# Kernel tuning notes

Measured on AMD Instinct MI355X. Metric: run time of the kernel, lower is better.

The kernel has to match this reference:

```python
import jax, jax.numpy as jnp
import numpy as np
from jax import lax

VOCAB, EMB, HID, TAGS = 8000, 300, 512, 24  # hidden_dim=512 -> 256 per direction
B, S = 128, 512
H2 = HID // 2


def setup_inputs() -> dict:
    key = jax.random.key(0)
    ks = jax.random.split(key, 16)
    sc = 0.05
    inp = {
        "chars": jax.random.randint(ks[0], (B, S), 0, VOCAB),
        "tags": jax.random.randint(ks[1], (B, S), 0, TAGS),
        "mask": jnp.ones((B, S), dtype=bool),
        "emb": jax.random.normal(ks[2], (VOCAB, EMB), jnp.float32) * sc,
        # PyTorch LSTM layout: gates stacked [i, f, g, o]
        "w_ih_f": jax.random.normal(ks[3], (4 * H2, EMB), jnp.float32) * sc,
        "w_hh_f": jax.random.normal(ks[4], (4 * H2, H2), jnp.float32) * sc,
        "b_f": jax.random.normal(ks[5], (4 * H2,), jnp.float32) * sc,  # b_ih + b_hh fused
        "w_ih_b": jax.random.normal(ks[6], (4 * H2, EMB), jnp.float32) * sc,
        "w_hh_b": jax.random.normal(ks[7], (4 * H2, H2), jnp.float32) * sc,
        "b_b": jax.random.normal(ks[8], (4 * H2,), jnp.float32) * sc,
        "w_out": jax.random.normal(ks[9], (TAGS, HID), jnp.float32) * sc,
        "b_out": jax.random.normal(ks[10], (TAGS,), jnp.float32) * sc,
        "trans": jax.random.normal(ks[11], (TAGS, TAGS), jnp.float32) * sc,
        "start_trans": jax.random.normal(ks[12], (TAGS,), jnp.float32) * sc,
        "end_trans": jax.random.normal(ks[13], (TAGS,), jnp.float32) * sc,
    }
    return inp


def _lstm_dir(x, w_ih, w_hh, b, reverse):
    # x: [B, S, E] -> h: [B, S, H2]
    gx = jnp.einsum('bse,ge->bsg', x, w_ih) + b  # [B, S, 4*H2]

    def step(carry, g_t):
        h, c = carry
        g = g_t + h @ w_hh.T
        i, f, gg, o = jnp.split(g, 4, axis=-1)
        c = jax.nn.sigmoid(f) * c + jax.nn.sigmoid(i) * jnp.tanh(gg)
        h = jax.nn.sigmoid(o) * jnp.tanh(c)
        return (h, c), h

    init = (jnp.zeros((x.shape[0], H2), x.dtype), jnp.zeros((x.shape[0], H2), x.dtype))
    _, hs = lax.scan(step, init, jnp.swapaxes(gx, 0, 1), reverse=reverse)
    return jnp.swapaxes(hs, 0, 1)


def _crf_loss(emissions, tags, mask, trans, start_trans, end_trans):
    # torchcrf log-likelihood, reduction='mean'; loss = -mean
    b, s, t = emissions.shape
    maskf = mask.astype(emissions.dtype)
    # numerator: score of gold path
    em_t = jnp.take_along_axis(emissions, tags[..., None], axis=2)[..., 0]  # [B,S]
    tr_t = trans[tags[:, :-1], tags[:, 1:]]  # [B,S-1]
    score = start_trans[tags[:, 0]] + em_t[:, 0]
    score = score + jnp.sum((em_t[:, 1:] + tr_t) * maskf[:, 1:], axis=1)
    seq_ends = jnp.sum(mask.astype(jnp.int32), axis=1) - 1  # [B]
    last_tags = jnp.take_along_axis(tags, seq_ends[:, None], axis=1)[:, 0]
    score = score + end_trans[last_tags]
    # denominator: forward algorithm via scan
    alpha0 = start_trans + emissions[:, 0]  # [B,T]

    def step(alpha, inputs):
        em, m = inputs  # em [B,T], m [B]
        nxt = jax.nn.logsumexp(alpha[:, :, None] + trans[None] + em[:, None, :], axis=1)
        alpha = jnp.where(m[:, None], nxt, alpha)
        return alpha, None

    alpha, _ = lax.scan(step, alpha0,
                        (jnp.swapaxes(emissions[:, 1:], 0, 1), jnp.swapaxes(mask[:, 1:], 0, 1)))
    log_z = jax.nn.logsumexp(alpha + end_trans, axis=1)  # [B]
    llh = score - log_z
    return -jnp.mean(llh)


def reference(chars, tags, mask, emb, w_ih_f, w_hh_f, b_f, w_ih_b, w_hh_b, b_b,
              w_out, b_out, trans, start_trans, end_trans):
    x = emb[chars]  # [B,S,E]
    h_f = _lstm_dir(x, w_ih_f, w_hh_f, b_f, reverse=False)
    h_b = _lstm_dir(x, w_ih_b, w_hh_b, b_b, reverse=True)
    lstm_out = jnp.concatenate([h_f, h_b], axis=-1)  # [B,S,HID]
    emissions = jnp.einsum('bsh,th->bst', lstm_out, w_out) + b_out  # [B,S,TAGS]
    return _crf_loss(emissions, tags, mask, trans, start_trans, end_trans)
```

## Files before the change

kernel.cpp:

```cpp
#include <hip/hip_runtime.h>
#include <math.h>

#define BB   128
#define SS   512
#define EMBD 300
#define VOC  8000
#define NTAG 24
#define BSD  (BB*SS)

#define SW   400.0f
#define SH   512.0f
#define INVQ (1.0f / (400.0f * 512.0f))

typedef unsigned int   u32;
typedef unsigned short u16;
typedef unsigned char  u8;

__device__ __forceinline__ int idot4(u32 a, u32 b, int c) {
#if __has_builtin(__builtin_amdgcn_sdot4)
    return __builtin_amdgcn_sdot4((int)a, (int)b, c, false);
#else
    int s = c;
    #pragma unroll
    for (int e = 0; e < 4; ++e) {
        int xa = ((int)(a << (24 - 8 * e))) >> 24;
        int xb = ((int)(b << (24 - 8 * e))) >> 24;
        s += xa * xb;
    }
    return s;
#endif
}
__device__ __forceinline__ u32 rdlane(u32 v, int l) {
#if __has_builtin(__builtin_amdgcn_readlane)
    return (u32)__builtin_amdgcn_readlane((int)v, l);
#else
    return (u32)__shfl((int)v, l);
#endif
}
__device__ __forceinline__ void bar_lds() {
    asm volatile("s_waitcnt lgkmcnt(0)" ::: "memory");
    __builtin_amdgcn_s_barrier();
}
__device__ __forceinline__ float sigm(float x) { return 1.0f / (1.0f + __expf(-x)); }
__device__ __forceinline__ float tanh_fast(float x) {
    return 1.0f - 2.0f / (__expf(2.0f * x) + 1.0f);
}
__device__ __forceinline__ int qclamp(float x, float s) {
    int v = (int)rintf(x * s);
    return v > 127 ? 127 : (v < -127 ? -127 : v);
}
__device__ __forceinline__ u32 q4(const float* p, float s) {
    u32 r = 0;
    #pragma unroll
    for (int e = 0; e < 4; ++e)
        r |= ((u32)(qclamp(p[e], s) & 0xFF)) << (8 * e);
    return r;
}

__global__ __launch_bounds__(512)
void k_packW(const float* __restrict__ w_hh_f, const float* __restrict__ w_hh_b,
             const float* __restrict__ w_out,
             u32* __restrict__ wreg, uint4* __restrict__ wlds,
             uint4* __restrict__ wstr, u32* __restrict__ woq)
{
    const int dir = blockIdx.x;
    const int t   = threadIdx.x;
    const float* w = dir ? w_hh_b : w_hh_f;
    const float* rowA = w + (size_t)t * 256;
    const float* rowB = w + (size_t)(t + 512) * 256;

    for (int q = 0; q < 16; ++q) {
        wreg[((size_t)(dir * 32 + q) * 512) + t]      = q4(rowA + 4 * q, SW);
        wreg[((size_t)(dir * 32 + 16 + q) * 512) + t] = q4(rowB + 4 * q, SW);
    }
    for (int qq = 0; qq < 7; ++qq) {
        uint4 va, vb;
        va.x = q4(rowA + 4 * (16 + 4 * qq + 0), SW);
        va.y = q4(rowA + 4 * (16 + 4 * qq + 1), SW);
        va.z = q4(rowA + 4 * (16 + 4 * qq + 2), SW);
        va.w = q4(rowA + 4 * (16 + 4 * qq + 3), SW);
        vb.x = q4(rowB + 4 * (16 + 4 * qq + 0), SW);
        vb.y = q4(rowB + 4 * (16 + 4 * qq + 1), SW);
        vb.z = q4(rowB + 4 * (16 + 4 * qq + 2), SW);
        vb.w = q4(rowB + 4 * (16 + 4 * qq + 3), SW);
        wlds[((size_t)(dir * 14 + qq) * 512) + t]     = va;
        wlds[((size_t)(dir * 14 + 7 + qq) * 512) + t] = vb;
    }
    for (int qq = 0; qq < 5; ++qq) {
        uint4 va, vb;
        va.x = q4(rowA + 4 * (44 + 4 * qq + 0), SW);
        va.y = q4(rowA + 4 * (44 + 4 * qq + 1), SW);
        va.z = q4(rowA + 4 * (44 + 4 * qq + 2), SW);
        va.w = q4(rowA + 4 * (44 + 4 * qq + 3), SW);
        vb.x = q4(rowB + 4 * (44 + 4 * qq + 0), SW);
        vb.y = q4(rowB + 4 * (44 + 4 * qq + 1), SW);
        vb.z = q4(rowB + 4 * (44 + 4 * qq + 2), SW);
        vb.w = q4(rowB + 4 * (44 + 4 * qq + 3), SW);
        wstr[((size_t)(dir * 10 + qq) * 512) + t]     = va;
        wstr[((size_t)(dir * 10 + 5 + qq) * 512) + t] = vb;
    }
    for (int i = t; i < NTAG * 64; i += 512) {
        const int tag = i >> 6, q = i & 63;
        woq[(size_t)dir * NTAG * 64 + i] =
            q4(w_out + (size_t)tag * 512 + dir * 256 + 4 * q, SW);
    }
}

__global__ __launch_bounds__(256)
void k_gxtab(const float* __restrict__ emb,
             const float* __restrict__ w_f, const float* __restrict__ bias_f,
             const float* __restrict__ w_b, const float* __restrict__ bias_b,
             u16* __restrict__ gxtab)
{
    const int dir = blockIdx.z;
    const float* W    = dir ? w_b    : w_f;
    const float* bias = dir ? bias_b : bias_f;
    u16* out = gxtab + (size_t)dir * VOC * 1024;
    const int r0 = blockIdx.y * 64;
    const int c0 = blockIdx.x * 128;

    __shared__ float As[16][65];
    __shared__ float Bs[16][129];

    const int tid = threadIdx.x;
    const int kk = tid & 15;
    const int rr = tid >> 4;
    const int ty = tid >> 4;
    const int tx = tid & 15;

    float acc[4][8] = {};

    for (int kt = 0; kt < EMBD; kt += 16) {
        const int k = kt + kk;
        const bool kok = (k < EMBD);
        #pragma unroll
        for (int p = 0; p < 4; ++p)
            As[kk][rr + p * 16] = kok ? emb[(size_t)(r0 + rr + p * 16) * EMBD + k] : 0.0f;
        #pragma unroll
        for (int p = 0; p < 8; ++p)
            Bs[kk][rr + p * 16] = kok ? W[(size_t)(c0 + rr + p * 16) * EMBD + k] : 0.0f;
        __syncthreads();
        #pragma unroll
        for (int q = 0; q < 16; ++q) {
            float av[4], bv[8];
            #pragma unroll
            for (int i = 0; i < 4; ++i) av[i] = As[q][ty * 4 + i];
            #pragma unroll
            for (int jj = 0; jj < 8; ++jj) bv[jj] = Bs[q][jj * 16 + tx];
            #pragma unroll
            for (int i = 0; i < 4; ++i)
                #pragma unroll
                for (int jj = 0; jj < 8; ++jj)
                    acc[i][jj] = fmaf(av[i], bv[jj], acc[i][jj]);
        }
        __syncthreads();
    }

    #pragma unroll
    for (int i = 0; i < 4; ++i) {
        const size_t rb = (size_t)(r0 + ty * 4 + i) * 1024;
        #pragma unroll
        for (int jj = 0; jj < 8; ++jj) {
            const int cl = c0 + jj * 16 + tx;
            out[rb + cl] = __builtin_bit_cast(u16, (_Float16)(acc[i][jj] + bias[cl]));
        }
    }
}

__global__ __launch_bounds__(512, 2)
void k_lstm_rl(const int* __restrict__ chars, const u16* __restrict__ gxtab,
               const u32* __restrict__ wreg, const uint4* __restrict__ wlds,
               const uint4* __restrict__ wstr,
               u32* __restrict__ hst)
{
    const int bid = blockIdx.x;
    const int dir = bid >> 7;
    const int b   = bid & 127;
    const int tid = threadIdx.x;

    __shared__ __align__(16) uint4 ldsW[14 * 512];
    __shared__ __align__(16) u32   hq[2][64];
    __shared__ __align__(16) float2 xg[256];
    __shared__ int chlds[SS];

    chlds[tid] = chars[(size_t)b * SS + tid];
    {
        const uint4* wl = wlds + (size_t)dir * 14 * 512;
        #pragma unroll
        for (int q = 0; q < 14; ++q) ldsW[q * 512 + tid] = wl[(size_t)q * 512 + tid];
    }

    u32 WR[32];
    {
        const u32* wrp = wreg + (size_t)dir * 32 * 512 + tid;
        #pragma unroll
        for (int q = 0; q < 32; ++q) WR[q] = wrp[(size_t)q * 512];
    }
    const uint4* wsp = wstr + (size_t)dir * 10 * 512 + tid;

    const u16* gxp = gxtab + (size_t)dir * VOC * 1024;

    float c = 0.0f;
    u32 hreg = 0u;
    __syncthreads();

    const int t0 = dir ? (SS - 1) : 0;
    u16 gA = gxp[(size_t)chlds[t0] * 1024 + tid];
    u16 gB = gxp[(size_t)chlds[t0] * 1024 + 512 + tid];

    int cur = 0;
    #pragma unroll 1
    for (int sloc = 0; sloc < SS; ++sloc) {
        const int t = dir ? (SS - 1 - sloc) : sloc;

        u16 gA_n = 0, gB_n = 0;
        if (sloc < SS - 1) {
            const int tn = dir ? (t - 1) : (t + 1);
            const size_t o = (size_t)chlds[tn] * 1024 + tid;
            gA_n = gxp[o];
            gB_n = gxp[o + 512];
        }
        uint4 s[10];
        #pragma unroll
        for (int qq = 0; qq < 10; ++qq) s[qq] = wsp[(size_t)qq * 512];

        int aA = 0, aB = 0;
        #pragma unroll
        for (int q = 0; q < 16; ++q) {
            const u32 hs = rdlane(hreg, q);
            aA = idot4(WR[q], hs, aA);
            aB = idot4(WR[16 + q], hs, aB);
        }
        #pragma unroll
        for (int qq = 0; qq < 7; ++qq) {
            const uint4 wa = ldsW[qq * 512 + tid];
            const uint4 wb = ldsW[(7 + qq) * 512 + tid];
            const u32 h0 = rdlane(hreg, 16 + 4 * qq + 0);
            const u32 h1 = rdlane(hreg, 16 + 4 * qq + 1);
            const u32 h2 = rdlane(hreg, 16 + 4 * qq + 2);
            const u32 h3 = rdlane(hreg, 16 + 4 * qq + 3);
            aA = idot4(wa.x, h0, aA); aB = idot4(wb.x, h0, aB);
            aA = idot4(wa.y, h1, aA); aB = idot4(wb.y, h1, aB);
            aA = idot4(wa.z, h2, aA); aB = idot4(wb.z, h2, aB);
            aA = idot4(wa.w, h3, aA); aB = idot4(wb.w, h3, aB);
        }
        #pragma unroll
        for (int qq = 0; qq < 5; ++qq) {
            const uint4 wa = s[qq];
            const uint4 wb = s[5 + qq];
            const u32 h0 = rdlane(hreg, 44 + 4 * qq + 0);
            const u32 h1 = rdlane(hreg, 44 + 4 * qq + 1);
            const u32 h2 = rdlane(hreg, 44 + 4 * qq + 2);
            const u32 h3 = rdlane(hreg, 44 + 4 * qq + 3);
            aA = idot4(wa.x, h0, aA); aB = idot4(wb.x, h0, aB);
            aA = idot4(wa.y, h1, aA); aB = idot4(wb.y, h1, aB);
            aA = idot4(wa.z, h2, aA); aB = idot4(wb.z, h2, aB);
            aA = idot4(wa.w, h3, aA); aB = idot4(wb.w, h3, aB);
        }
        const float apreA = (float)aA * INVQ + (float)__builtin_bit_cast(_Float16, gA);
        const float apreB = (float)aB * INVQ + (float)__builtin_bit_cast(_Float16, gB);

        if (tid >= 256) xg[tid - 256] = make_float2(sigm(apreA), sigm(apreB));
        bar_lds();

        if (tid < 256) {
            const float2 fo = xg[tid];
            const float ig = sigm(apreA);
            const float gg = tanh_fast(apreB);
            c = fmaf(fo.x, c, ig * gg);
            const float h = fo.y * tanh_fast(c);
            const int hi = qclamp(h, SH);
            ((u8*)hq[cur ^ 1])[tid] = (u8)(hi & 0xFF);
        }
        bar_lds();

        hreg = hq[cur ^ 1][tid & 63];
        if (tid < 64)
            hst[(((size_t)b * SS + t) * 2 + dir) * 64 + tid] = hreg;

        gA = gA_n; gB = gB_n;
        cur ^= 1;
    }
}

__global__ __launch_bounds__(256)
void k_emis(const u32* __restrict__ hst, const u32* __restrict__ woq,
            const float* __restrict__ b_out, float* __restrict__ emis)
{
    const int r0  = blockIdx.x * 32;
    const int tid = threadIdx.x;

    __shared__ __align__(16) u32 hs[32 * 132];
    __shared__ __align__(16) u32 wo[NTAG * 132];

    #pragma unroll
    for (int p = 0; p < 16; ++p) {
        const int idx = p * 256 + tid;
        const int row = idx >> 7, rest = idx & 127;
        hs[row * 132 + rest] = hst[((size_t)(r0 + row)) * 128 + rest];
    }
    for (int i = tid; i < NTAG * 128; i += 256) {
        const int tag = i >> 7, q = i & 127;
        const u32 v = (q < 64) ? woq[tag * 64 + q]
                               : woq[NTAG * 64 + tag * 64 + (q - 64)];
        wo[tag * 132 + q] = v;
    }
    __syncthreads();

    #pragma unroll
    for (int rep = 0; rep < 3; ++rep) {
        const int out = rep * 256 + tid;
        const int row = out / 24;
        const int tag = out - row * 24;
        const uint4* h4 = (const uint4*)&hs[row * 132];
        const uint4* w4 = (const uint4*)&wo[tag * 132];
        int e = 0;
        #pragma unroll
        for (int q = 0; q < 32; ++q) {
            const uint4 hv = h4[q];
            const uint4 wv = w4[q];
            e = idot4(wv.x, hv.x, e);
            e = idot4(wv.y, hv.y, e);
            e = idot4(wv.z, hv.z, e);
            e = idot4(wv.w, hv.w, e);
        }
        emis[(size_t)(r0 + row) * NTAG + tag] = (float)e * INVQ + b_out[tag];
    }
}

__global__ __launch_bounds__(64)
void k_crf(const float* __restrict__ emis, const int* __restrict__ tags,
           const float* __restrict__ trans, const float* __restrict__ start_tr,
           const float* __restrict__ end_tr, float* __restrict__ llh)
{
    const int b    = blockIdx.x;
    const int lane = threadIdx.x;
    const float* em = emis + (size_t)b * SS * NTAG;
    const int*   tg = tags + (size_t)b * SS;
    const bool active = (lane < NTAG);

    float trans_reg[NTAG];
    #pragma unroll
    for (int i = 0; i < NTAG; ++i)
        trans_reg[i] = active ? trans[i * NTAG + lane] : 0.0f;

    float sc = 0.0f;
    for (int t = lane; t < SS; t += 64) {
        const int tt = tg[t];
        sc += em[t * NTAG + tt];
        if (t > 0) sc += trans[tg[t - 1] * NTAG + tt];
    }
    #pragma unroll
    for (int off = 32; off > 0; off >>= 1) sc += __shfl_down(sc, off);

    float alpha = active ? (start_tr[lane] + em[lane]) : -1e30f;
    for (int t = 1; t < SS; ++t) {
        float v[NTAG];
        #pragma unroll
        for (int i = 0; i < NTAG; ++i)
            v[i] = __shfl(alpha, i) + trans_reg[i];
        float m = v[0];
        #pragma unroll
        for (int i = 1; i < NTAG; ++i) m = fmaxf(m, v[i]);
        float ssum = 0.0f;
        #pragma unroll
        for (int i = 0; i < NTAG; ++i) ssum += __expf(v[i] - m);
        const float e = active ? em[t * NTAG + lane] : 0.0f;
        alpha = active ? (m + __logf(ssum) + e) : -1e30f;
    }

    float v = alpha + (active ? end_tr[lane] : 0.0f);
    float m = v;
    #pragma unroll
    for (int off = 32; off > 0; off >>= 1) m = fmaxf(m, __shfl_down(m, off));
    m = __shfl(m, 0);
    float e = __expf(v - m);
    #pragma unroll
    for (int off = 32; off > 0; off >>= 1) e += __shfl_down(e, off);

    if (lane == 0) {
        const float logz  = m + __logf(e);
        const float score = sc + start_tr[tg[0]] + end_tr[tg[SS - 1]];
        llh[b] = score - logz;
    }
}

__global__ __launch_bounds__(64)
void k_final(const float* __restrict__ llh, float* __restrict__ out)
{
    const int lane = threadIdx.x;
    float v = llh[lane] + llh[lane + 64];
    #pragma unroll
    for (int off = 32; off > 0; off >>= 1) v += __shfl_down(v, off);
    if (lane == 0) out[0] = -(v * (1.0f / 128.0f));
}

extern "C" void kernel_launch(void* const* d_in, const int* in_sizes, int n_in,
                              void* d_out, int out_size, void* d_ws, size_t ws_size,
                              hipStream_t stream)
{
    (void)in_sizes; (void)n_in; (void)out_size; (void)ws_size;

    const int*   chars   = (const int*)d_in[0];
    const int*   tags    = (const int*)d_in[1];
    const float* emb     = (const float*)d_in[3];
    const float* w_ih_f  = (const float*)d_in[4];
    const float* w_hh_f  = (const float*)d_in[5];
    const float* b_f     = (const float*)d_in[6];
    const float* w_ih_b  = (const float*)d_in[7];
    const float* w_hh_b  = (const float*)d_in[8];
    const float* b_b     = (const float*)d_in[9];
    const float* w_out   = (const float*)d_in[10];
    const float* b_out   = (const float*)d_in[11];
    const float* trans   = (const float*)d_in[12];
    const float* start_t = (const float*)d_in[13];
    const float* end_t   = (const float*)d_in[14];

    char* ws = (char*)d_ws;
    size_t off = 0;
    auto carve = [&](size_t bytes) -> char* {
        char* p = ws + off;
        off += (bytes + 255) & ~(size_t)255;
        return p;
    };
    u16*   gxtab  = (u16*)carve((size_t)2 * VOC * 1024 * 2);
    u32*   wreg   = (u32*)carve((size_t)2 * 32 * 512 * 4);
    uint4* wlds   = (uint4*)carve((size_t)2 * 14 * 512 * 16);
    uint4* wstr   = (uint4*)carve((size_t)2 * 10 * 512 * 16);
    u32*   woq    = (u32*)carve((size_t)2 * NTAG * 64 * 4);
    u32*   hst    = (u32*)carve((size_t)BSD * 2 * 64 * 4);
    float* emis   = (float*)carve((size_t)BSD * NTAG * 4);
    float* llh    = (float*)carve(128 * 4);

    hipLaunchKernelGGL(k_packW, dim3(2), dim3(512), 0, stream,
                       w_hh_f, w_hh_b, w_out, wreg, wlds, wstr, woq);
    hipLaunchKernelGGL(k_gxtab, dim3(8, 125, 2), dim3(256), 0, stream,
                       emb, w_ih_f, b_f, w_ih_b, b_b, gxtab);
    hipLaunchKernelGGL(k_lstm_rl, dim3(256), dim3(512), 0, stream,
                       chars, gxtab, wreg, wlds, wstr, hst);
    hipLaunchKernelGGL(k_emis, dim3(BSD / 32), dim3(256), 0, stream,
                       hst, woq, b_out, emis);
    hipLaunchKernelGGL(k_crf, dim3(128), dim3(64), 0, stream,
                       emis, tags, trans, start_t, end_t, llh);
    hipLaunchKernelGGL(k_final, dim3(1), dim3(64), 0, stream,
                       llh, (float*)d_out);
}
```

Measured before the change: 1.107 ms.

## Use 1024-thread LSTM blocks with one gate per thread and int8 input GEMM

The recurrent kernel moves from 512 threads computing two gate rows each to 1024 threads computing one gate row each. Each thread keeps 44 weight words in registers and reads the other 20 words from LDS, so the per-step global streaming of weights is dropped. The embedding and input-weight GEMM is rewritten to quantise inputs to int8 in a new pack kernel and accumulate with sdot4. This shortens the serial dependency chain per step and cuts the precompute cost, at the price of extra quantisation error in the input projection and heavier register and occupancy pressure.

After: 1.126 ms. No clear change (+1.7%).

```diff
diff --git a/kernel.cpp b/kernel.cpp
--- a/kernel.cpp
+++ b/kernel.cpp
@@ -8,9 +8,16 @@
 #define NTAG 24
 #define BSD  (BB*SS)
 
+#define RKG  44
+#define LKG  5
+
 #define SW   400.0f
 #define SH   512.0f
 #define INVQ (1.0f / (400.0f * 512.0f))
+
+#define SQE  440.0f
+#define INVQE (1.0f / (440.0f * 440.0f))
+#define KQ   80
 
 typedef unsigned int   u32;
 typedef unsigned short u16;
@@ -56,48 +63,54 @@
         r |= ((u32)(qclamp(p[e], s) & 0xFF)) << (8 * e);
     return r;
 }
+__device__ __forceinline__ u32 q4g(const float* p, int n, float s) {
+    u32 r = 0;
+    #pragma unroll
+    for (int e = 0; e < 4; ++e) {
+        const int v = (e < n) ? qclamp(p[e], s) : 0;
+        r |= ((u32)(v & 0xFF)) << (8 * e);
+    }
+    return r;
+}
+
+__global__ __launch_bounds__(128)
+void k_packE(const float* __restrict__ emb, const float* __restrict__ w_ih_f,
+             const float* __restrict__ w_ih_b, u32* __restrict__ eq)
+{
+    const int row = blockIdx.x;
+    const int g   = threadIdx.x;
+    if (g >= KQ) return;
+    const float* src = (row < 8000) ? (emb + (size_t)row * EMBD)
+                     : (row < 9024) ? (w_ih_f + (size_t)(row - 8000) * EMBD)
+                                    : (w_ih_b + (size_t)(row - 9024) * EMBD);
+    const int ks = g * 4;
+    const int n  = (ks >= EMBD) ? 0 : ((EMBD - ks) >= 4 ? 4 : (EMBD - ks));
+    eq[(size_t)row * KQ + g] = (n == 4) ? q4(src + ks, SQE) : q4g(src + ks, n, SQE);
+}
 
 __global__ __launch_bounds__(512)
 void k_packW(const float* __restrict__ w_hh_f, const float* __restrict__ w_hh_b,
              const float* __restrict__ w_out,
              u32* __restrict__ wreg, uint4* __restrict__ wlds,
-             uint4* __restrict__ wstr, u32* __restrict__ woq)
+             u32* __restrict__ woq)
 {
     const int dir = blockIdx.x;
     const int t   = threadIdx.x;
     const float* w = dir ? w_hh_b : w_hh_f;
-    const float* rowA = w + (size_t)t * 256;
-    const float* rowB = w + (size_t)(t + 512) * 256;
-
-    for (int q = 0; q < 16; ++q) {
-        wreg[((size_t)(dir * 32 + q) * 512) + t]      = q4(rowA + 4 * q, SW);
-        wreg[((size_t)(dir * 32 + 16 + q) * 512) + t] = q4(rowB + 4 * q, SW);
-    }
-    for (int qq = 0; qq < 7; ++qq) {
-        uint4 va, vb;
-        va.x = q4(rowA + 4 * (16 + 4 * qq + 0), SW);
-        va.y = q4(rowA + 4 * (16 + 4 * qq + 1), SW);
-        va.z = q4(rowA + 4 * (16 + 4 * qq + 2), SW);
-        va.w = q4(rowA + 4 * (16 + 4 * qq + 3), SW);
-        vb.x = q4(rowB + 4 * (16 + 4 * qq + 0), SW);
-        vb.y = q4(rowB + 4 * (16 + 4 * qq + 1), SW);
-        vb.z = q4(rowB + 4 * (16 + 4 * qq + 2), SW);
-        vb.w = q4(rowB + 4 * (16 + 4 * qq + 3), SW);
-        wlds[((size_t)(dir * 14 + qq) * 512) + t]     = va;
-        wlds[((size_t)(dir * 14 + 7 + qq) * 512) + t] = vb;
-    }
-    for (int qq = 0; qq < 5; ++qq) {
-        uint4 va, vb;
-        va.x = q4(rowA + 4 * (44 + 4 * qq + 0), SW);
-        va.y = q4(rowA + 4 * (44 + 4 * qq + 1), SW);
-        va.z = q4(rowA + 4 * (44 + 4 * qq + 2), SW);
-        va.w = q4(rowA + 4 * (44 + 4 * qq + 3), SW);
-        vb.x = q4(rowB + 4 * (44 + 4 * qq + 0), SW);
-        vb.y = q4(rowB + 4 * (44 + 4 * qq + 1), SW);
-        vb.z = q4(rowB + 4 * (44 + 4 * qq + 2), SW);
-        vb.w = q4(rowB + 4 * (44 + 4 * qq + 3), SW);
-        wstr[((size_t)(dir * 10 + qq) * 512) + t]     = va;
-        wstr[((size_t)(dir * 10 + 5 + qq) * 512) + t] = vb;
+
+    for (int half = 0; half < 2; ++half) {
+        const int r = half * 512 + t;
+        const float* row = w + (size_t)r * 256;
+        for (int q = 0; q < RKG; ++q)
+            wreg[((size_t)(dir * RKG + q) * 1024) + r] = q4(row + 4 * q, SW);
+        for (int qq = 0; qq < LKG; ++qq) {
+            uint4 v;
+            v.x = q4(row + 4 * (RKG + 4 * qq + 0), SW);
+            v.y = q4(row + 4 * (RKG + 4 * qq + 1), SW);
+            v.z = q4(row + 4 * (RKG + 4 * qq + 2), SW);
+            v.w = q4(row + 4 * (RKG + 4 * qq + 3), SW);
+            wlds[((size_t)(dir * LKG + qq) * 1024) + r] = v;
+        }
     }
     for (int i = t; i < NTAG * 64; i += 512) {
         const int tag = i >> 6, q = i & 63;
@@ -107,42 +120,51 @@
 }
 
 __global__ __launch_bounds__(256)
-void k_gxtab(const float* __restrict__ emb,
-             const float* __restrict__ w_f, const float* __restrict__ bias_f,
-             const float* __restrict__ w_b, const float* __restrict__ bias_b,
+void k_gxtab(const u32* __restrict__ eq,
+             const float* __restrict__ bias_f, const float* __restrict__ bias_b,
              u16* __restrict__ gxtab)
 {
     const int dir = blockIdx.z;
-    const float* W    = dir ? w_b    : w_f;
     const float* bias = dir ? bias_b : bias_f;
     u16* out = gxtab + (size_t)dir * VOC * 1024;
     const int r0 = blockIdx.y * 64;
     const int c0 = blockIdx.x * 128;
 
-    __shared__ float As[16][65];
-    __shared__ float Bs[16][129];
+    const u32* A = eq + (size_t)r0 * KQ;
+    const u32* B = eq + (size_t)(8000 + dir * 1024 + c0) * KQ;
+
+    __shared__ u32 As[16][66];
+    __shared__ u32 Bs[16][130];
 
     const int tid = threadIdx.x;
-    const int kk = tid & 15;
-    const int rr = tid >> 4;
     const int ty = tid >> 4;
     const int tx = tid & 15;
 
-    float acc[4][8] = {};
-
-    for (int kt = 0; kt < EMBD; kt += 16) {
-        const int k = kt + kk;
-        const bool kok = (k < EMBD);
-        #pragma unroll
-        for (int p = 0; p < 4; ++p)
-            As[kk][rr + p * 16] = kok ? emb[(size_t)(r0 + rr + p * 16) * EMBD + k] : 0.0f;
-        #pragma unroll
-        for (int p = 0; p < 8; ++p)
-            Bs[kk][rr + p * 16] = kok ? W[(size_t)(c0 + rr + p * 16) * EMBD + k] : 0.0f;
+    int acc[4][8] = {};
+
+    for (int kt = 0; kt < 5; ++kt) {
+        {
+            const int r = tid >> 2, qd = tid & 3;
+            const uint4 v = *(const uint4*)&A[(size_t)r * KQ + kt * 16 + qd * 4];
+            As[qd * 4 + 0][r] = v.x;
+            As[qd * 4 + 1][r] = v.y;
+            As[qd * 4 + 2][r] = v.z;
+            As[qd * 4 + 3][r] = v.w;
+        }
+        #pragma unroll
+        for (int e = 0; e < 2; ++e) {
+            const int idx = tid * 2 + e;
+            const int r = idx >> 2, qd = idx & 3;
+            const uint4 v = *(const uint4*)&B[(size_t)r * KQ + kt * 16 + qd * 4];
+            Bs[qd * 4 + 0][r] = v.x;
+            Bs[qd * 4 + 1][r] = v.y;
+            Bs[qd * 4 + 2][r] = v.z;
+            Bs[qd * 4 + 3][r] = v.w;
+        }
         __syncthreads();
         #pragma unroll
         for (int q = 0; q < 16; ++q) {
-            float av[4], bv[8];
+            u32 av[4], bv[8];
             #pragma unroll
             for (int i = 0; i < 4; ++i) av[i] = As[q][ty * 4 + i];
             #pragma unroll
@@ -151,7 +173,7 @@
             for (int i = 0; i < 4; ++i)
                 #pragma unroll
                 for (int jj = 0; jj < 8; ++jj)
-                    acc[i][jj] = fmaf(av[i], bv[jj], acc[i][jj]);
+                    acc[i][jj] = idot4(av[i], bv[jj], acc[i][jj]);
         }
         __syncthreads();
     }
@@ -162,15 +184,15 @@
         #pragma unroll
         for (int jj = 0; jj < 8; ++jj) {
             const int cl = c0 + jj * 16 + tx;
-            out[rb + cl] = __builtin_bit_cast(u16, (_Float16)(acc[i][jj] + bias[cl]));
-        }
-    }
-}
-
-__global__ __launch_bounds__(512, 2)
-void k_lstm_rl(const int* __restrict__ chars, const u16* __restrict__ gxtab,
+            const float v = (float)acc[i][jj] * INVQE + bias[cl];
+            out[rb + cl] = __builtin_bit_cast(u16, (_Float16)v);
+        }
+    }
+}
+
+__global__ __launch_bounds__(1024)
+void k_lstm_1k(const int* __restrict__ chars, const u16* __restrict__ gxtab,
                const u32* __restrict__ wreg, const uint4* __restrict__ wlds,
-               const uint4* __restrict__ wstr,
                u32* __restrict__ hst)
 {
     const int bid = blockIdx.x;
@@ -178,25 +200,25 @@
     const int b   = bid & 127;
     const int tid = threadIdx.x;
 
-    __shared__ __align__(16) uint4 ldsW[14 * 512];
+    __shared__ __align__(16) uint4 ldsW[LKG * 1024];
     __shared__ __align__(16) u32   hq[2][64];
-    __shared__ __align__(16) float2 xg[256];
+    __shared__ __align__(16) float xg[768];
     __shared__ int chlds[SS];
 
-    chlds[tid] = chars[(size_t)b * SS + tid];
+    if (tid < SS) chlds[tid] = chars[(size_t)b * SS + tid];
     {
-        const uint4* wl = wlds + (size_t)dir * 14 * 512;
-        #pragma unroll
-        for (int q = 0; q < 14; ++q) ldsW[q * 512 + tid] = wl[(size_t)q * 512 + tid];
-    }
-
-    u32 WR[32];
+        const uint4* wl = wlds + (size_t)dir * LKG * 1024;
+        #pragma unroll
+        for (int q = 0; q < LKG; ++q) ldsW[q * 1024 + tid] = wl[(size_t)q * 1024 + tid];
+    }
+    if (tid < 64) { hq[0][tid] = 0u; hq[1][tid] = 0u; }
+
+    u32 WR[RKG];
     {
-        const u32* wrp = wreg + (size_t)dir * 32 * 512 + tid;
-        #pragma unroll
-        for (int q = 0; q < 32; ++q) WR[q] = wrp[(size_t)q * 512];
-    }
-    const uint4* wsp = wstr + (size_t)dir * 10 * 512 + tid;
+        const u32* wrp = wreg + (size_t)dir * RKG * 1024 + tid;
+        #pragma unroll
+        for (int q = 0; q < RKG; ++q) WR[q] = wrp[(size_t)q * 1024];
+    }
 
     const u16* gxp = gxtab + (size_t)dir * VOC * 1024;
 
@@ -206,71 +228,47 @@
 
     const int t0 = dir ? (SS - 1) : 0;
     u16 gA = gxp[(size_t)chlds[t0] * 1024 + tid];
-    u16 gB = gxp[(size_t)chlds[t0] * 1024 + 512 + tid];
 
     int cur = 0;
     #pragma unroll 1
     for (int sloc = 0; sloc < SS; ++sloc) {
         const int t = dir ? (SS - 1 - sloc) : sloc;
 
-        u16 gA_n = 0, gB_n = 0;
+        u16 gA_n = 0;
         if (sloc < SS - 1) {
             const int tn = dir ? (t - 1) : (t + 1);
-            const size_t o = (size_t)chlds[tn] * 1024 + tid;
-            gA_n = gxp[o];
-            gB_n = gxp[o + 512];
-        }
-        uint4 s[10];
-        #pragma unroll
-        for (int qq = 0; qq < 10; ++qq) s[qq] = wsp[(size_t)qq * 512];
-
-        int aA = 0, aB = 0;
-        #pragma unroll
-        for (int q = 0; q < 16; ++q) {
-            const u32 hs = rdlane(hreg, q);
-            aA = idot4(WR[q], hs, aA);
-            aB = idot4(WR[16 + q], hs, aB);
-        }
-        #pragma unroll
-        for (int qq = 0; qq < 7; ++qq) {
-            const uint4 wa = ldsW[qq * 512 + tid];
-            const uint4 wb = ldsW[(7 + qq) * 512 + tid];
-            const u32 h0 = rdlane(hreg, 16 + 4 * qq + 0);
-            const u32 h1 = rdlane(hreg, 16 + 4 * qq + 1);
-            const u32 h2 = rdlane(hreg, 16 + 4 * qq + 2);
-            const u32 h3 = rdlane(hreg, 16 + 4 * qq + 3);
-            aA = idot4(wa.x, h0, aA); aB = idot4(wb.x, h0, aB);
-            aA = idot4(wa.y, h1, aA); aB = idot4(wb.y, h1, aB);
-            aA = idot4(wa.z, h2, aA); aB = idot4(wb.z, h2, aB);
-            aA = idot4(wa.w, h3, aA); aB = idot4(wb.w, h3, aB);
-        }
-        #pragma unroll
-        for (int qq = 0; qq < 5; ++qq) {
-            const uint4 wa = s[qq];
-            const uint4 wb = s[5 + qq];
-            const u32 h0 = rdlane(hreg, 44 + 4 * qq + 0);
-            const u32 h1 = rdlane(hreg, 44 + 4 * qq + 1);
-            const u32 h2 = rdlane(hreg, 44 + 4 * qq + 2);
-            const u32 h3 = rdlane(hreg, 44 + 4 * qq + 3);
-            aA = idot4(wa.x, h0, aA); aB = idot4(wb.x, h0, aB);
-            aA = idot4(wa.y, h1, aA); aB = idot4(wb.y, h1, aB);
-            aA = idot4(wa.z, h2, aA); aB = idot4(wb.z, h2, aB);
-            aA = idot4(wa.w, h3, aA); aB = idot4(wb.w, h3, aB);
-        }
-        const float apreA = (float)aA * INVQ + (float)__builtin_bit_cast(_Float16, gA);
-        const float apreB = (float)aB * INVQ + (float)__builtin_bit_cast(_Float16, gB);
-
-        if (tid >= 256) xg[tid - 256] = make_float2(sigm(apreA), sigm(apreB));
+            gA_n = gxp[(size_t)chlds[tn] * 1024 + tid];
+        }
+
+        int a0 = 0, a1 = 0;
+        #pragma unroll
+        for (int q = 0; q < RKG; q += 2) {
+            a0 = idot4(WR[q],     rdlane(hreg, q),     a0);
+            a1 = idot4(WR[q + 1], rdlane(hreg, q + 1), a1);
+        }
+        #pragma unroll
+        for (int qq = 0; qq < LKG; ++qq) {
+            const uint4 wv = ldsW[qq * 1024 + tid];
+            a0 = idot4(wv.x, rdlane(hreg, RKG + 4 * qq + 0), a0);
+            a1 = idot4(wv.y, rdlane(hreg, RKG + 4 * qq + 1), a1);
+            a0 = idot4(wv.z, rdlane(hreg, RKG + 4 * qq + 2), a0);
+            a1 = idot4(wv.w, rdlane(hreg, RKG + 4 * qq + 3), a1);
+        }
+        const float apre = (float)(a0 + a1) * INVQ
+                         + (float)__builtin_bit_cast(_Float16, gA);
+
+        if (tid >= 768)      xg[tid - 256] = sigm(apre);
+        else if (tid >= 512) xg[tid - 256] = tanh_fast(apre);
+        else if (tid >= 256) xg[tid - 256] = sigm(apre);
         bar_lds();
 
         if (tid < 256) {
-            const float2 fo = xg[tid];
-            const float ig = sigm(apreA);
-            const float gg = tanh_fast(apreB);
-            c = fmaf(fo.x, c, ig * gg);
-            const float h = fo.y * tanh_fast(c);
-            const int hi = qclamp(h, SH);
-            ((u8*)hq[cur ^ 1])[tid] = (u8)(hi & 0xFF);
+            const float fg = xg[tid];
+            const float gg = xg[tid + 256];
+            const float og = xg[tid + 512];
+            c = fmaf(fg, c, sigm(apre) * gg);
+            const float h = og * tanh_fast(c);
+            ((u8*)hq[cur ^ 1])[tid] = (u8)(qclamp(h, SH) & 0xFF);
         }
         bar_lds();
 
@@ -278,7 +276,7 @@
         if (tid < 64)
             hst[(((size_t)b * SS + t) * 2 + dir) * 64 + tid] = hreg;
 
-        gA = gA_n; gB = gB_n;
+        gA = gA_n;
         cur ^= 1;
     }
 }
@@ -424,20 +422,22 @@
         return p;
     };
     u16*   gxtab  = (u16*)carve((size_t)2 * VOC * 1024 * 2);
-    u32*   wreg   = (u32*)carve((size_t)2 * 32 * 512 * 4);
-    uint4* wlds   = (uint4*)carve((size_t)2 * 14 * 512 * 16);
-    uint4* wstr   = (uint4*)carve((size_t)2 * 10 * 512 * 16);
+    u32*   eq     = (u32*)carve((size_t)10048 * KQ * 4);
+    u32*   wreg   = (u32*)carve((size_t)2 * RKG * 1024 * 4);
+    uint4* wlds   = (uint4*)carve((size_t)2 * LKG * 1024 * 16);
     u32*   woq    = (u32*)carve((size_t)2 * NTAG * 64 * 4);
     u32*   hst    = (u32*)carve((size_t)BSD * 2 * 64 * 4);
     float* emis   = (float*)carve((size_t)BSD * NTAG * 4);
     float* llh    = (float*)carve(128 * 4);
 
+    hipLaunchKernelGGL(k_packE, dim3(10048), dim3(128), 0, stream,
+                       emb, w_ih_f, w_ih_b, eq);
     hipLaunchKernelGGL(k_packW, dim3(2), dim3(512), 0, stream,
-                       w_hh_f, w_hh_b, w_out, wreg, wlds, wstr, woq);
+                       w_hh_f, w_hh_b, w_out, wreg, wlds, woq);
     hipLaunchKernelGGL(k_gxtab, dim3(8, 125, 2), dim3(256), 0, stream,
-                       emb, w_ih_f, b_f, w_ih_b, b_b, gxtab);
-    hipLaunchKernelGGL(k_lstm_rl, dim3(256), dim3(512), 0, stream,
-                       chars, gxtab, wreg, wlds, wstr, hst);
+                       eq, b_f, b_b, gxtab);
+    hipLaunchKernelGGL(k_lstm_1k, dim3(256), dim3(1024), 0, stream,
+                       chars, gxtab, wreg, wlds, hst);
     hipLaunchKernelGGL(k_emis, dim3(BSD / 32), dim3(256), 0, stream,
                        hst, woq, b_out, emis);
     hipLaunchKernelGGL(k_crf, dim3(128), dim3(64), 0, stream,
```
